# Optimization experiments

Measured on AMD Instinct MI355X. Metric: run time of the kernel, lower is better.

## Reference

```python
import jax, jax.numpy as jnp
import numpy as np

TEMPERATURE = 1.0


def setup_inputs() -> dict:
    key = jax.random.key(0)
    k1, k2, k3, k4, k5 = jax.random.split(key, 5)
    B, D, Da, Dv = 8192, 128, 64, 64
    return {
        "a_features": jax.random.normal(k1, (B, D), dtype=jnp.float32),
        "v_features": jax.random.normal(k2, (B, D), dtype=jnp.float32),
        "audio_only_indices": jax.random.randint(k3, (Da,), 0, D, dtype=jnp.int64),
        "image_only_indices": jax.random.randint(k4, (Dv,), 0, D, dtype=jnp.int64),
        "labels": jax.random.randint(k5, (B,), 0, 10, dtype=jnp.int64),
    }


def reference(a_features, v_features, audio_only_indices, image_only_indices, labels):
    # Gather modality-specific feature subspaces: [B, Da] / [B, Dv]
    audio_only = a_features[:, audio_only_indices]          # a-features, audio dims
    image_audio_only = v_features[:, audio_only_indices]    # v-features, audio dims
    image_only = v_features[:, image_only_indices]          # v-features, image dims
    audio_image_only = a_features[:, image_only_indices]    # a-features, image dims

    # Per original: the dot-product partner is detached (stop_gradient).
    # v_loss_i = -log( exp(<v_i, a_i>/T) / sum_j exp(<v_i, a_j>/T) )
    #          = logsumexp_j(S_v[i, j]) - S_v[i, i]
    S_v = jnp.matmul(image_audio_only,
                     jax.lax.stop_gradient(audio_only).T) / TEMPERATURE  # [B, B]
    S_a = jnp.matmul(audio_image_only,
                     jax.lax.stop_gradient(image_only).T) / TEMPERATURE  # [B, B]

    v_loss = jnp.mean(jax.nn.logsumexp(S_v, axis=1) - jnp.diagonal(S_v))
    a_loss = jnp.mean(jax.nn.logsumexp(S_a, axis=1) - jnp.diagonal(S_a))
    return v_loss + a_loss
```

## Files before the change

### kernel.cpp

```cpp
#include <hip/hip_runtime.h>
#include <hip/hip_bf16.h>

typedef __attribute__((ext_vector_type(8))) short bf16x8;
typedef __attribute__((ext_vector_type(4))) float f32x4;

#define BN 8192
#define DF 128
#define DG 64
static constexpr float L2E = 1.44269504088896340736f;
static constexpr float LN2 = 0.69314718055994530942f;

__device__ __forceinline__ size_t frag_off(int row, int d) {
  int tile = row >> 4, m = row & 15;
  int half = d >> 5, q = (d >> 3) & 3, c = d & 7;
  return (size_t)tile * 1024 + (size_t)half * 512 + (size_t)(q * 16 + m) * 8 + c;
}

__global__ __launch_bounds__(256) void gather_k(
    const float* __restrict__ a, const float* __restrict__ v,
    const int* __restrict__ aidx, const int* __restrict__ iidx,
    __hip_bfloat16* __restrict__ Xv, __hip_bfloat16* __restrict__ Ya,
    __hip_bfloat16* __restrict__ Xa, __hip_bfloat16* __restrict__ Yv,
    float* __restrict__ diag, float* __restrict__ rowsum,
    float* __restrict__ out) {
  int tid = threadIdx.x;
  int gid = blockIdx.x * 256 + tid;
  if (gid < 2 * BN) rowsum[gid] = 0.f;
  if (gid == 0) out[0] = 0.f;

  int lane = tid & 63;
  int row  = blockIdx.x * 4 + (tid >> 6);
  int ka = aidx[lane];
  int ki = iidx[lane];
  float va = v[row * DF + ka];
  float aa = a[row * DF + ka];
  float ai = a[row * DF + ki];
  float vi = v[row * DF + ki];
  size_t fo = frag_off(row, lane);
  Xv[fo] = __float2bfloat16(va * L2E);
  Ya[fo] = __float2bfloat16(aa);
  Xa[fo] = __float2bfloat16(ai * L2E);
  Yv[fo] = __float2bfloat16(vi);

  float dv = va * aa;
  float da = ai * vi;
#pragma unroll
  for (int off = 32; off >= 1; off >>= 1) {
    dv += __shfl_xor(dv, off);
    da += __shfl_xor(da, off);
  }
  if (lane == 0) {
    diag[row]      = dv;
    diag[BN + row] = da;
  }
}

__global__ __launch_bounds__(256, 4) void lse_main(
    const unsigned short* __restrict__ Xv, const unsigned short* __restrict__ Ya,
    const unsigned short* __restrict__ Xa, const unsigned short* __restrict__ Yv,
    float* __restrict__ rowsum) {
  const unsigned short* X;
  const unsigned short* Y;
  float* rs;
  if (blockIdx.z == 0) { X = Xv; Y = Ya; rs = rowsum; }
  else                 { X = Xa; Y = Yv; rs = rowsum + BN; }

  int tid  = threadIdx.x;
  int lane = tid & 63;
  int m = lane & 15;
  int q = lane >> 4;
  int row0 = blockIdx.x * 256 + (tid >> 6) * 64;

  bf16x8 af[4][2];
#pragma unroll
  for (int t = 0; t < 4; ++t) {
    const unsigned short* p =
        X + (size_t)(row0 / 16 + t) * 1024 + (size_t)lane * 8;
    af[t][0] = *(const bf16x8*)p;
    af[t][1] = *(const bf16x8*)(p + 512);
  }

  float part[4][4] = {};
  const f32x4 zero = {0.f, 0.f, 0.f, 0.f};

  const unsigned short* bbase =
      Y + (size_t)(blockIdx.y * 32) * 1024 + (size_t)lane * 8;
  bf16x8 b0 = *(const bf16x8*)bbase;
  bf16x8 b1 = *(const bf16x8*)(bbase + 512);

#pragma unroll 2
  for (int jt = 0; jt < 32; ++jt) {
    int jn = (jt < 31) ? jt + 1 : 31;
    const unsigned short* np = bbase + (size_t)jn * 1024;
    bf16x8 n0 = *(const bf16x8*)np;
    bf16x8 n1 = *(const bf16x8*)(np + 512);
#pragma unroll
    for (int t = 0; t < 4; ++t) {
      f32x4 c = __builtin_amdgcn_mfma_f32_16x16x32_bf16(af[t][0], b0, zero, 0, 0, 0);
      c = __builtin_amdgcn_mfma_f32_16x16x32_bf16(af[t][1], b1, c, 0, 0, 0);
      part[t][0] += __builtin_amdgcn_exp2f(c[0]);
      part[t][1] += __builtin_amdgcn_exp2f(c[1]);
      part[t][2] += __builtin_amdgcn_exp2f(c[2]);
      part[t][3] += __builtin_amdgcn_exp2f(c[3]);
    }
    b0 = n0;
    b1 = n1;
  }

#pragma unroll
  for (int off = 1; off < 16; off <<= 1) {
#pragma unroll
    for (int t = 0; t < 4; ++t)
#pragma unroll
      for (int r = 0; r < 4; ++r)
        part[t][r] += __shfl_xor(part[t][r], off);
  }
  if (m == 0) {
#pragma unroll
    for (int t = 0; t < 4; ++t)
#pragma unroll
      for (int r = 0; r < 4; ++r)
        atomicAdd(&rs[row0 + t * 16 + q * 4 + r], part[t][r]);
  }
}

__global__ __launch_bounds__(256) void finalize_k(
    const float* __restrict__ rowsum, const float* __restrict__ diag,
    float* __restrict__ out) {
  int i = blockIdx.x * 256 + threadIdx.x;
  float local = LN2 * __builtin_amdgcn_logf(rowsum[i]) - diag[i];
#pragma unroll
  for (int off = 32; off >= 1; off >>= 1) local += __shfl_xor(local, off);
  __shared__ float red[4];
  int wave = threadIdx.x >> 6;
  if ((threadIdx.x & 63) == 0) red[wave] = local;
  __syncthreads();
  if (threadIdx.x == 0) {
    float bs = red[0] + red[1] + red[2] + red[3];
    atomicAdd(out, bs * (1.f / (float)BN));
  }
}

extern "C" void kernel_launch(void* const* d_in, const int* in_sizes, int n_in,
                              void* d_out, int out_size, void* d_ws, size_t ws_size,
                              hipStream_t stream) {
  const float* a   = (const float*)d_in[0];
  const float* v   = (const float*)d_in[1];
  const int* aidx  = (const int*)d_in[2];
  const int* iidx  = (const int*)d_in[3];

  char* ws = (char*)d_ws;
  const size_t MB = 1024 * 1024;
  __hip_bfloat16* Xv = (__hip_bfloat16*)(ws + 0 * MB);
  __hip_bfloat16* Ya = (__hip_bfloat16*)(ws + 1 * MB);
  __hip_bfloat16* Xa = (__hip_bfloat16*)(ws + 2 * MB);
  __hip_bfloat16* Yv = (__hip_bfloat16*)(ws + 3 * MB);
  float* diag   = (float*)(ws + 4 * MB);
  float* rowsum = (float*)(ws + 4 * MB + 64 * 1024);

  gather_k<<<BN / 4, 256, 0, stream>>>(a, v, aidx, iidx, Xv, Ya, Xa, Yv,
                                       diag, rowsum, (float*)d_out);
  lse_main<<<dim3(BN / 256, 16, 2), 256, 0, stream>>>(
      (const unsigned short*)Xv, (const unsigned short*)Ya,
      (const unsigned short*)Xa, (const unsigned short*)Yv, rowsum);
  finalize_k<<<64, 256, 0, stream>>>(rowsum, diag, (float*)d_out);
}
```

Before: 92.93 us.

## Coalesce gather loads with shuffles, drop occupancy hint and unroll pragma

The gather kernel now reads each feature row with coalesced float2 loads and picks the indexed columns with wave shuffles, replacing scattered per-lane global loads. In the main kernel the min-blocks-per-CU launch bound and the unroll-2 pragma are removed, and the partial sums are held as f32x4 vectors so the adds can be packed. The hint removal lets the compiler use more registers at the cost of possible occupancy loss, and the shuffle path adds extra cross-lane instructions.

```diff
diff --git a/kernel.cpp b/kernel.cpp
--- a/kernel.cpp
+++ b/kernel.cpp
@@ -32,10 +32,19 @@
   int row  = blockIdx.x * 4 + (tid >> 6);
   int ka = aidx[lane];
   int ki = iidx[lane];
-  float va = v[row * DF + ka];
-  float aa = a[row * DF + ka];
-  float ai = a[row * DF + ki];
-  float vi = v[row * DF + ki];
+
+  float2 a2 = ((const float2*)(a + (size_t)row * DF))[lane];
+  float2 v2 = ((const float2*)(v + (size_t)row * DF))[lane];
+
+  float axa = __shfl(a2.x, ka >> 1), aya = __shfl(a2.y, ka >> 1);
+  float vxa = __shfl(v2.x, ka >> 1), vya = __shfl(v2.y, ka >> 1);
+  float axi = __shfl(a2.x, ki >> 1), ayi = __shfl(a2.y, ki >> 1);
+  float vxi = __shfl(v2.x, ki >> 1), vyi = __shfl(v2.y, ki >> 1);
+  float aa = (ka & 1) ? aya : axa;
+  float va = (ka & 1) ? vya : vxa;
+  float ai = (ki & 1) ? ayi : axi;
+  float vi = (ki & 1) ? vyi : vxi;
+
   size_t fo = frag_off(row, lane);
   Xv[fo] = __float2bfloat16(va * L2E);
   Ya[fo] = __float2bfloat16(aa);
@@ -55,7 +64,7 @@
   }
 }
 
-__global__ __launch_bounds__(256, 4) void lse_main(
+__global__ __launch_bounds__(256) void lse_main(
     const unsigned short* __restrict__ Xv, const unsigned short* __restrict__ Ya,
     const unsigned short* __restrict__ Xa, const unsigned short* __restrict__ Yv,
     float* __restrict__ rowsum) {
@@ -80,7 +89,7 @@
     af[t][1] = *(const bf16x8*)(p + 512);
   }
 
-  float part[4][4] = {};
+  f32x4 part[4] = {};
   const f32x4 zero = {0.f, 0.f, 0.f, 0.f};
 
   const unsigned short* bbase =
@@ -88,7 +97,6 @@
   bf16x8 b0 = *(const bf16x8*)bbase;
   bf16x8 b1 = *(const bf16x8*)(bbase + 512);
 
-#pragma unroll 2
   for (int jt = 0; jt < 32; ++jt) {
     int jn = (jt < 31) ? jt + 1 : 31;
     const unsigned short* np = bbase + (size_t)jn * 1024;
@@ -98,10 +106,12 @@
     for (int t = 0; t < 4; ++t) {
       f32x4 c = __builtin_amdgcn_mfma_f32_16x16x32_bf16(af[t][0], b0, zero, 0, 0, 0);
       c = __builtin_amdgcn_mfma_f32_16x16x32_bf16(af[t][1], b1, c, 0, 0, 0);
-      part[t][0] += __builtin_amdgcn_exp2f(c[0]);
-      part[t][1] += __builtin_amdgcn_exp2f(c[1]);
-      part[t][2] += __builtin_amdgcn_exp2f(c[2]);
-      part[t][3] += __builtin_amdgcn_exp2f(c[3]);
+      f32x4 e;
+      e[0] = __builtin_amdgcn_exp2f(c[0]);
+      e[1] = __builtin_amdgcn_exp2f(c[1]);
+      e[2] = __builtin_amdgcn_exp2f(c[2]);
+      e[3] = __builtin_amdgcn_exp2f(c[3]);
+      part[t] += e;
     }
     b0 = n0;
     b1 = n1;
@@ -110,10 +120,11 @@
 #pragma unroll
   for (int off = 1; off < 16; off <<= 1) {
 #pragma unroll
-    for (int t = 0; t < 4; ++t)
+    for (int t = 0; t < 4; ++t) {
 #pragma unroll
       for (int r = 0; r < 4; ++r)
         part[t][r] += __shfl_xor(part[t][r], off);
+    }
   }
   if (m == 0) {
 #pragma unroll
```

Result: slower. 94.81 us (+2.0%).
